# Kernel optimization log

Measured on AMD Instinct MI355X. Metric: run time of the kernel, lower is better.

The kernel has to match this reference:

```python
import jax, jax.numpy as jnp
import numpy as np

B, L, H, LAB = 64, 128, 512, 128

def setup_inputs() -> dict:
    key = jax.random.key(0)
    ks = jax.random.split(key, 8)
    s = 1.0 / np.sqrt(H)  # PyTorch LSTM/Linear uniform bound as a std-ish scale
    return {
        "x": jax.random.normal(ks[0], (B, L, 2 * H), jnp.float32),
        "hi": jax.random.normal(ks[1], (B, L, 2 * H), jnp.float32),
        "W_ih": jax.random.normal(ks[2], (4 * H, 5 * H), jnp.float32) * s,
        "W_hh": jax.random.normal(ks[3], (4 * H, H), jnp.float32) * s,
        "b_ih": jax.random.normal(ks[4], (4 * H,), jnp.float32) * s,
        "b_hh": jax.random.normal(ks[5], (4 * H,), jnp.float32) * s,
        "W_fc": jax.random.normal(ks[6], (LAB, H), jnp.float32) * s,
        "b_fc": jax.random.normal(ks[7], (LAB,), jnp.float32) * s,
    }

def _cell(xi, h, c, W_ih, W_hh, b_ih, b_hh):
    # PyTorch LSTMCell math, gate order: input, forget, cell(g), output
    gates = xi @ W_ih.T + b_ih + h @ W_hh.T + b_hh  # [4H]
    i, f, g, o = jnp.split(gates, 4)
    i = jax.nn.sigmoid(i); f = jax.nn.sigmoid(f); o = jax.nn.sigmoid(o)
    g = jnp.tanh(g)
    c = f * c + i * g
    h = o * jnp.tanh(c)
    return h, c

def reference(x, hi, W_ih, W_hh, b_ih, b_hh, W_fc, b_fc):
    Bm, Lm, _ = x.shape
    Hm = W_hh.shape[1]
    xs = jnp.concatenate([x, hi], axis=-1).transpose(1, 0, 2)  # [L, B, 4H]
    # Faithful to the torch code: nn.LSTM (batch_first=False) is fed [B,1,5H]
    # with state (1,1,H), so it scans the batch dim as 'time' with a single
    # shared (h,c) that also persists across outer timesteps.
    def time_step(carry, x_t):
        h, c, prev_out = carry  # h,c: [H]; prev_out: [B,H] (outputs of prev t)
        inp = jnp.concatenate([x_t, prev_out], axis=-1)  # [B, 5H]
        def batch_step(hc, xi):
            hh, cc = hc
            hh, cc = _cell(xi, hh, cc, W_ih, W_hh, b_ih, b_hh)
            return (hh, cc), hh
        (h, c), outs = jax.lax.scan(batch_step, (h, c), inp)  # outs: [B,H]
        return (h, c, outs), outs
    init = (jnp.zeros((Hm,), x.dtype), jnp.zeros((Hm,), x.dtype),
            jnp.zeros((Bm, Hm), x.dtype))
    _, all_out = jax.lax.scan(time_step, init, xs)  # [L, B, H]
    output = all_out.transpose(1, 0, 2)  # [B, L, H]
    return output @ W_fc.T + b_fc  # [B, L, label_size]
```

## Files before the change

### kernel.cpp

```cpp
#include <hip/hip_runtime.h>
#include <stdint.h>


#define HDIM   512
#define NSTEP  8192
#define GATES  2048
#define XDIM   2048
#define IN5H   2560
#define LSEQ   128
#define LAB    128
#define SPIN_LIMIT 1000000

typedef float f32x4 __attribute__((ext_vector_type(4)));
typedef short bf16x8 __attribute__((ext_vector_type(8)));

__device__ __forceinline__ unsigned f2bf(float v){
  unsigned u = __float_as_uint(v);
  u += 0x7fffu + ((u >> 16) & 1u);
  return u >> 16;
}
__device__ __forceinline__ float bf2f_lo(unsigned lo){ return __uint_as_float((lo & 0xffffu) << 16); }
__device__ __forceinline__ float bf2f_hi(unsigned lo){ return __uint_as_float(lo & 0xffff0000u); }

template<int PREMODE>
__global__ __launch_bounds__(256) void gemm_pre(
    const float* __restrict__ x, const float* __restrict__ hi,
    const float* __restrict__ Wih, const float* __restrict__ bih,
    const float* __restrict__ bhh, void* __restrict__ preOut)
{
  __shared__ unsigned short As[128][40];
  __shared__ unsigned short Bs[128][40];
  const int tid = threadIdx.x;
  const int bm = blockIdx.x, bn = blockIdx.y;
  const int lane = tid & 63, wv = tid >> 6;
  const int wm = wv & 1, wn = wv >> 1;

  const int srow = tid >> 1;
  const int ch   = (tid & 1) * 16;

  const int gr = bm*128 + srow;
  const int bb = gr & 63, tt = gr >> 6;
  const float* ax = x  + (size_t)(bb*LSEQ + tt) * 1024;
  const float* ah = hi + (size_t)(bb*LSEQ + tt) * 1024;
  const int R = bn*128 + srow;
  const float* bw = Wih + (size_t)R * IN5H;

  f32x4 acc[4][4];
  #pragma unroll
  for (int m=0;m<4;++m)
    #pragma unroll
    for (int n=0;n<4;++n) acc[m][n] = (f32x4){0.f,0.f,0.f,0.f};

  for (int kc = 0; kc < XDIM; kc += 32){
    const int c0 = kc + ch;
    const float* ap = (c0 < 1024) ? (ax + c0) : (ah + (c0 - 1024));
    #pragma unroll
    for (int q=0;q<4;++q){
      float4 va = *(const float4*)(ap + 4*q);
      float4 vb = *(const float4*)(bw + c0 + 4*q);
      ushort4 ua; ua.x=f2bf(va.x); ua.y=f2bf(va.y); ua.z=f2bf(va.z); ua.w=f2bf(va.w);
      ushort4 ub; ub.x=f2bf(vb.x); ub.y=f2bf(vb.y); ub.z=f2bf(vb.z); ub.w=f2bf(vb.w);
      *(ushort4*)&As[srow][ch + 4*q] = ua;
      *(ushort4*)&Bs[srow][ch + 4*q] = ub;
    }
    __syncthreads();
    bf16x8 afr[4], bfr[4];
    const int mr = wm*64 + (lane & 15);
    const int nr = wn*64 + (lane & 15);
    const int ko = (lane >> 4) * 8;
    #pragma unroll
    for (int m=0;m<4;++m) afr[m] = *(const bf16x8*)&As[mr + 16*m][ko];
    #pragma unroll
    for (int n=0;n<4;++n) bfr[n] = *(const bf16x8*)&Bs[nr + 16*n][ko];
    #pragma unroll
    for (int m=0;m<4;++m)
      #pragma unroll
      for (int n=0;n<4;++n)
        acc[m][n] = __builtin_amdgcn_mfma_f32_16x16x32_bf16(afr[m], bfr[n], acc[m][n], 0, 0, 0);
    __syncthreads();
  }
  #pragma unroll
  for (int n=0;n<4;++n){
    const int scol = bn*128 + wn*64 + 16*n + (lane & 15);
    const float bias = bih[scol] + bhh[scol];
    #pragma unroll
    for (int m=0;m<4;++m){
      const int sr0 = bm*128 + wm*64 + 16*m + (lane >> 4)*4;
      #pragma unroll
      for (int q=0;q<4;++q){
        const float v = acc[m][n][q] + bias;
        if (PREMODE == 0){
          ((float*)preOut)[(size_t)(sr0 + q) * GATES + scol] = v;
        } else {
          const float vn = __shfl_xor(v, 1, 64);
          if (!(lane & 1)){
            const unsigned word = f2bf(v) | (f2bf(vn) << 16);
            ((unsigned*)preOut)[(size_t)(sr0 + q) * 1024 + (scol >> 1)] = word;
          }
        }
      }
    }
  }
}

template<int PREMODE>
__global__ __launch_bounds__(512) void lstm_seq(
    const float* __restrict__ Wih, const float* __restrict__ Whh,
    const void* __restrict__ preOut, unsigned long long* __restrict__ units)
{
  const int tid = threadIdx.x;
  const int w = blockIdx.x;
  const int k = tid >> 6, l = tid & 63;

  __shared__ float hvec[512];
  __shared__ float uvec[512];
  __shared__ float accS[32];
  __shared__ float accU[32];
  __shared__ float preBuf[2][32];
  __shared__ int   sDead;

  float wu[4][8], wh[4][8];
  #pragma unroll
  for (int i=0;i<4;++i){
    const int rl = 4*k + i;
    const int gate = rl >> 3, jl = rl & 7;
    const int R = gate*HDIM + 8*w + jl;
    const float* pu = Wih + (size_t)R*IN5H + XDIM;
    const float* ph = Whh + (size_t)R*HDIM;
    #pragma unroll
    for (int c=0;c<8;++c){ wu[i][c] = pu[l + 64*c]; wh[i][c] = ph[l + 64*c]; }
  }
  hvec[tid] = 0.f; uvec[tid] = 0.f;
  if (tid == 0) sDead = 0;
  if (tid < 32) accU[tid] = 0.f;
  if (tid >= 32 && tid < 64){
    const int rl = tid - 32;
    if (PREMODE == 0){
      preBuf[0][rl] = ((const float*)preOut)[(size_t)0*GATES + (rl >> 3)*HDIM + 8*w + (rl & 7)];
    } else if (rl < 16){
      const int g = rl >> 2, wi = rl & 3;
      const unsigned word = ((const unsigned*)preOut)[(size_t)0*1024 + g*256 + 4*w + wi];
      preBuf[0][2*rl]   = bf2f_lo(word);
      preBuf[0][2*rl+1] = bf2f_hi(word);
    }
  }
  float cst = 0.f;
  __syncthreads();

  for (int s = 0; s < NSTEP; ++s){
    const int dead = sDead;
    if (!dead){
      if (k < 4){
        if (s > 0){
          const int idx = k*64 + l;
          const unsigned long long* p = units + (size_t)(s-1)*256 + idx;
          unsigned long long v; int trips = 0; int ok;
          do {
            v = __hip_atomic_load(p, __ATOMIC_RELAXED, __HIP_MEMORY_SCOPE_AGENT);
            ok = __all((int)((unsigned)(v >> 32) == (unsigned)s));
          } while (!ok && ++trips < SPIN_LIMIT);
          if (!ok) sDead = 1;
          const unsigned lo = (unsigned)v;
          hvec[2*idx]   = bf2f_lo(lo);
          hvec[2*idx+1] = bf2f_hi(lo);
        }
      } else {
        if (s >= 63){
          const int idx = (k-4)*64 + l;
          const unsigned long long* p = units + (size_t)(s-63)*256 + idx;
          unsigned long long v; int trips = 0; int ok;
          do {
            v = __hip_atomic_load(p, __ATOMIC_RELAXED, __HIP_MEMORY_SCOPE_AGENT);
            ok = __all((int)((unsigned)(v >> 32) == (unsigned)(s-62)));
          } while (!ok && ++trips < SPIN_LIMIT);
          if (!ok) sDead = 1;
          const unsigned lo = (unsigned)v;
          uvec[2*idx]   = bf2f_lo(lo);
          uvec[2*idx+1] = bf2f_hi(lo);
        }
      }
    }
    __syncthreads();

    {
      float a0=0.f, a1=0.f, a2=0.f, a3=0.f;
      #pragma unroll
      for (int c=0;c<8;++c){
        const float hv = hvec[l + 64*c];
        a0 += wh[0][c]*hv; a1 += wh[1][c]*hv; a2 += wh[2][c]*hv; a3 += wh[3][c]*hv;
      }
      #pragma unroll
      for (int off=32; off>=1; off>>=1){
        a0 += __shfl_xor(a0, off, 64);
        a1 += __shfl_xor(a1, off, 64);
        a2 += __shfl_xor(a2, off, 64);
        a3 += __shfl_xor(a3, off, 64);
      }
      if (l == 0){
        accS[4*k+0] = a0 + accU[4*k+0];
        accS[4*k+1] = a1 + accU[4*k+1];
        accS[4*k+2] = a2 + accU[4*k+2];
        accS[4*k+3] = a3 + accU[4*k+3];
      }
    }
    __syncthreads();

    if (tid < 8){
      const int jl = tid;
      const float* pb = preBuf[s & 1];
      float gi = accS[jl]      + pb[jl];
      float gf = accS[8 + jl]  + pb[8 + jl];
      float gg = accS[16 + jl] + pb[16 + jl];
      float go = accS[24 + jl] + pb[24 + jl];
      gi = 1.f/(1.f + __expf(-gi));
      gf = 1.f/(1.f + __expf(-gf));
      go = 1.f/(1.f + __expf(-go));
      float e2 = __expf(2.f * fminf(fmaxf(gg, -15.f), 15.f));
      gg = (e2 - 1.f) / (e2 + 1.f);
      cst = gf*cst + gi*gg;
      float e2c = __expf(2.f * fminf(fmaxf(cst, -15.f), 15.f));
      const float hval = go * ((e2c - 1.f) / (e2c + 1.f));
      const float hn = __shfl_xor(hval, 1, 64);
      if ((jl & 1) == 0){
        const unsigned lo = f2bf(hval) | (f2bf(hn) << 16);
        const unsigned long long unit =
            (unsigned long long)lo | ((unsigned long long)(unsigned)(s + 1) << 32);
        __hip_atomic_store(units + (size_t)s*256 + (4*w + (jl >> 1)), unit,
                           __ATOMIC_RELAXED, __HIP_MEMORY_SCOPE_AGENT);
      }
    }
    {
      float a0=0.f, a1=0.f, a2=0.f, a3=0.f;
      #pragma unroll
      for (int c=0;c<8;++c){
        const float uv = uvec[l + 64*c];
        a0 += wu[0][c]*uv; a1 += wu[1][c]*uv; a2 += wu[2][c]*uv; a3 += wu[3][c]*uv;
      }
      #pragma unroll
      for (int off=32; off>=1; off>>=1){
        a0 += __shfl_xor(a0, off, 64);
        a1 += __shfl_xor(a1, off, 64);
        a2 += __shfl_xor(a2, off, 64);
        a3 += __shfl_xor(a3, off, 64);
      }
      if (l == 0){
        accU[4*k+0] = a0; accU[4*k+1] = a1; accU[4*k+2] = a2; accU[4*k+3] = a3;
      }
    }
    if ((s + 1) < NSTEP && tid >= 32 && tid < 64){
      const int rl = tid - 32;
      if (PREMODE == 0){
        preBuf[(s+1) & 1][rl] =
            ((const float*)preOut)[(size_t)(s+1)*GATES + (rl >> 3)*HDIM + 8*w + (rl & 7)];
      } else if (rl < 16){
        const int g = rl >> 2, wi = rl & 3;
        const unsigned word = ((const unsigned*)preOut)[(size_t)(s+1)*1024 + g*256 + 4*w + wi];
        preBuf[(s+1) & 1][2*rl]   = bf2f_lo(word);
        preBuf[(s+1) & 1][2*rl+1] = bf2f_hi(word);
      }
    }
    __syncthreads();
  }
}

__global__ __launch_bounds__(256) void fc_kernel(
    const unsigned long long* __restrict__ units,
    const float* __restrict__ Wfc, const float* __restrict__ bfc,
    float* __restrict__ out)
{
  __shared__ float hbuf[8][512];
  const int tid = threadIdx.x;
  const int s0 = blockIdx.x * 8;
  #pragma unroll
  for (int r=0;r<8;++r){
    const int q = tid + 256*r;
    const int si = q >> 8, u = q & 255;
    const unsigned lo = (unsigned)units[(size_t)(s0 + si)*256 + u];
    hbuf[si][2*u]   = bf2f_lo(lo);
    hbuf[si][2*u+1] = bf2f_hi(lo);
  }
  __syncthreads();
  const int lab = tid & 127, sg = tid >> 7;
  const float* wrow = Wfc + (size_t)lab * HDIM;
  const float bias = bfc[lab];
  for (int si = sg; si < 8; si += 2){
    float sum = 0.f;
    #pragma unroll 4
    for (int j=0;j<HDIM;j+=4){
      const float4 wv = *(const float4*)(wrow + j);
      sum += wv.x*hbuf[si][j] + wv.y*hbuf[si][j+1]
           + wv.z*hbuf[si][j+2] + wv.w*hbuf[si][j+3];
    }
    const int s = s0 + si;
    const int bb = s & 63, tt = s >> 6;
    out[((size_t)(bb*LSEQ + tt))*LAB + lab] = sum + bias;
  }
}

__global__ void sentinel_kernel(float* out, int n){
  const int i = blockIdx.x*256 + threadIdx.x;
  if (i < n) out[i] = 12345.0f;
}

extern "C" void kernel_launch(void* const* d_in, const int* in_sizes, int n_in,
                              void* d_out, int out_size, void* d_ws, size_t ws_size,
                              hipStream_t stream)
{
  const float* x   = (const float*)d_in[0];
  const float* hi  = (const float*)d_in[1];
  const float* Wih = (const float*)d_in[2];
  const float* Whh = (const float*)d_in[3];
  const float* bih = (const float*)d_in[4];
  const float* bhh = (const float*)d_in[5];
  const float* Wfc = (const float*)d_in[6];
  const float* bfc = (const float*)d_in[7];
  float* out = (float*)d_out;

  const size_t MB = 1024*1024;
  if (ws_size >= 80*MB){
    void* pre = d_ws;
    unsigned long long* units =
        (unsigned long long*)((char*)d_ws + 64*MB);
    gemm_pre<0><<<dim3(64, 16), 256, 0, stream>>>(x, hi, Wih, bih, bhh, pre);
    lstm_seq<0><<<64, 512, 0, stream>>>(Wih, Whh, pre, units);
    fc_kernel<<<1024, 256, 0, stream>>>(units, Wfc, bfc, out);
  } else if (ws_size >= 48*MB){
    void* pre = d_ws;
    unsigned long long* units =
        (unsigned long long*)((char*)d_ws + 32*MB);
    gemm_pre<1><<<dim3(64, 16), 256, 0, stream>>>(x, hi, Wih, bih, bhh, pre);
    lstm_seq<1><<<64, 512, 0, stream>>>(Wih, Whh, pre, units);
    fc_kernel<<<1024, 256, 0, stream>>>(units, Wfc, bfc, out);
  } else {
    sentinel_kernel<<<(out_size + 255)/256, 256, 0, stream>>>(out, out_size);
  }
}
```

Before: 17.67 ms.

## Give each wave one hidden unit and drop block barriers from the LSTM recurrence

Restructures the persistent LSTM kernel so each wavefront owns one hidden unit across all four gates. Each wave polls the flag-tagged h and u vectors directly into registers, reduces with shuffles and applies the gate math locally. This removes the three per-step __syncthreads and the shared-memory staging, and launches 128 blocks of 256 threads instead of 64 of 512. Each h entry becomes a 32-bit word holding a bf16 value and a 16-bit step tag, and the pre-activations are always stored as bf16. Every wave now loads the full vectors itself, which adds global/L2 traffic, and the 16-bit tag wraps at 65536 steps (fine for 8192 steps).

```diff
diff --git a/kernel.cpp b/kernel.cpp
--- a/kernel.cpp
+++ b/kernel.cpp
@@ -4,12 +4,11 @@
 
 #define HDIM   512
 #define NSTEP  8192
-#define GATES  2048
 #define XDIM   2048
 #define IN5H   2560
 #define LSEQ   128
 #define LAB    128
-#define SPIN_LIMIT 1000000
+#define SPIN_LIMIT 65536
 
 typedef float f32x4 __attribute__((ext_vector_type(4)));
 typedef short bf16x8 __attribute__((ext_vector_type(8)));
@@ -19,14 +18,13 @@
   u += 0x7fffu + ((u >> 16) & 1u);
   return u >> 16;
 }
-__device__ __forceinline__ float bf2f_lo(unsigned lo){ return __uint_as_float((lo & 0xffffu) << 16); }
-__device__ __forceinline__ float bf2f_hi(unsigned lo){ return __uint_as_float(lo & 0xffff0000u); }
-
-template<int PREMODE>
+__device__ __forceinline__ float bf2f_lo(unsigned w){ return __uint_as_float((w & 0xffffu) << 16); }
+__device__ __forceinline__ float bf2f_hi(unsigned w){ return __uint_as_float(w & 0xffff0000u); }
+
 __global__ __launch_bounds__(256) void gemm_pre(
     const float* __restrict__ x, const float* __restrict__ hi,
     const float* __restrict__ Wih, const float* __restrict__ bih,
-    const float* __restrict__ bhh, void* __restrict__ preOut)
+    const float* __restrict__ bhh, unsigned* __restrict__ pre32)
 {
   __shared__ unsigned short As[128][40];
   __shared__ unsigned short Bs[128][40];
@@ -89,182 +87,151 @@
       #pragma unroll
       for (int q=0;q<4;++q){
         const float v = acc[m][n][q] + bias;
-        if (PREMODE == 0){
-          ((float*)preOut)[(size_t)(sr0 + q) * GATES + scol] = v;
-        } else {
-          const float vn = __shfl_xor(v, 1, 64);
-          if (!(lane & 1)){
-            const unsigned word = f2bf(v) | (f2bf(vn) << 16);
-            ((unsigned*)preOut)[(size_t)(sr0 + q) * 1024 + (scol >> 1)] = word;
-          }
+        const float vn = __shfl_xor(v, 1, 64);
+        if (!(lane & 1)){
+          const unsigned word = f2bf(v) | (f2bf(vn) << 16);
+          pre32[(size_t)(sr0 + q) * 1024 + (scol >> 1)] = word;
         }
       }
     }
   }
 }
 
-template<int PREMODE>
-__global__ __launch_bounds__(512) void lstm_seq(
+__global__ __launch_bounds__(256, 1) void lstm_seq(
     const float* __restrict__ Wih, const float* __restrict__ Whh,
-    const void* __restrict__ preOut, unsigned long long* __restrict__ units)
+    const unsigned* __restrict__ pre32, unsigned* __restrict__ units)
 {
   const int tid = threadIdx.x;
-  const int w = blockIdx.x;
-  const int k = tid >> 6, l = tid & 63;
-
-  __shared__ float hvec[512];
-  __shared__ float uvec[512];
-  __shared__ float accS[32];
-  __shared__ float accU[32];
-  __shared__ float preBuf[2][32];
-  __shared__ int   sDead;
-
-  float wu[4][8], wh[4][8];
-  #pragma unroll
-  for (int i=0;i<4;++i){
-    const int rl = 4*k + i;
-    const int gate = rl >> 3, jl = rl & 7;
-    const int R = gate*HDIM + 8*w + jl;
-    const float* pu = Wih + (size_t)R*IN5H + XDIM;
-    const float* ph = Whh + (size_t)R*HDIM;
-    #pragma unroll
-    for (int c=0;c<8;++c){ wu[i][c] = pu[l + 64*c]; wh[i][c] = ph[l + 64*c]; }
-  }
-  hvec[tid] = 0.f; uvec[tid] = 0.f;
-  if (tid == 0) sDead = 0;
-  if (tid < 32) accU[tid] = 0.f;
-  if (tid >= 32 && tid < 64){
-    const int rl = tid - 32;
-    if (PREMODE == 0){
-      preBuf[0][rl] = ((const float*)preOut)[(size_t)0*GATES + (rl >> 3)*HDIM + 8*w + (rl & 7)];
-    } else if (rl < 16){
-      const int g = rl >> 2, wi = rl & 3;
-      const unsigned word = ((const unsigned*)preOut)[(size_t)0*1024 + g*256 + 4*w + wi];
-      preBuf[0][2*rl]   = bf2f_lo(word);
-      preBuf[0][2*rl+1] = bf2f_hi(word);
-    }
-  }
+  const int l = tid & 63;
+  const int j0 = blockIdx.x * 4 + (tid >> 6);
+
+  float wh[4][8], wu[4][8];
+  #pragma unroll
+  for (int g=0; g<4; ++g){
+    const float* ph = Whh + (size_t)(g*HDIM + j0)*HDIM;
+    const float* pu = Wih + (size_t)(g*HDIM + j0)*IN5H + XDIM;
+    #pragma unroll
+    for (int c=0; c<8; ++c){ wh[g][c] = ph[l + 64*c]; wu[g][c] = pu[l + 64*c]; }
+  }
+
+  const int phalf = j0 >> 1, psel = j0 & 1;
+  float pr[4];
+  #pragma unroll
+  for (int g=0; g<4; ++g){
+    const unsigned w0 = pre32[(size_t)0*1024 + g*256 + phalf];
+    pr[g] = psel ? bf2f_hi(w0) : bf2f_lo(w0);
+  }
+
   float cst = 0.f;
-  __syncthreads();
+  int dead = 0;
 
   for (int s = 0; s < NSTEP; ++s){
-    const int dead = sDead;
-    if (!dead){
-      if (k < 4){
-        if (s > 0){
-          const int idx = k*64 + l;
-          const unsigned long long* p = units + (size_t)(s-1)*256 + idx;
-          unsigned long long v; int trips = 0; int ok;
-          do {
-            v = __hip_atomic_load(p, __ATOMIC_RELAXED, __HIP_MEMORY_SCOPE_AGENT);
-            ok = __all((int)((unsigned)(v >> 32) == (unsigned)s));
-          } while (!ok && ++trips < SPIN_LIMIT);
-          if (!ok) sDead = 1;
-          const unsigned lo = (unsigned)v;
-          hvec[2*idx]   = bf2f_lo(lo);
-          hvec[2*idx+1] = bf2f_hi(lo);
-        }
+    float hv[8], uv[8];
+    if (s == 0){
+      #pragma unroll
+      for (int c=0;c<8;++c) hv[c] = 0.f;
+    } else {
+      const unsigned* bp = units + (size_t)(s-1)*HDIM + l;
+      unsigned v[8];
+      if (dead){
+        #pragma unroll
+        for (int c=0;c<8;++c) v[c] = __hip_atomic_load(bp + 64*c, __ATOMIC_RELAXED, __HIP_MEMORY_SCOPE_AGENT);
       } else {
-        if (s >= 63){
-          const int idx = (k-4)*64 + l;
-          const unsigned long long* p = units + (size_t)(s-63)*256 + idx;
-          unsigned long long v; int trips = 0; int ok;
-          do {
-            v = __hip_atomic_load(p, __ATOMIC_RELAXED, __HIP_MEMORY_SCOPE_AGENT);
-            ok = __all((int)((unsigned)(v >> 32) == (unsigned)(s-62)));
-          } while (!ok && ++trips < SPIN_LIMIT);
-          if (!ok) sDead = 1;
-          const unsigned lo = (unsigned)v;
-          uvec[2*idx]   = bf2f_lo(lo);
-          uvec[2*idx+1] = bf2f_hi(lo);
-        }
-      }
-    }
-    __syncthreads();
-
-    {
-      float a0=0.f, a1=0.f, a2=0.f, a3=0.f;
-      #pragma unroll
-      for (int c=0;c<8;++c){
-        const float hv = hvec[l + 64*c];
-        a0 += wh[0][c]*hv; a1 += wh[1][c]*hv; a2 += wh[2][c]*hv; a3 += wh[3][c]*hv;
-      }
-      #pragma unroll
-      for (int off=32; off>=1; off>>=1){
-        a0 += __shfl_xor(a0, off, 64);
-        a1 += __shfl_xor(a1, off, 64);
-        a2 += __shfl_xor(a2, off, 64);
-        a3 += __shfl_xor(a3, off, 64);
-      }
-      if (l == 0){
-        accS[4*k+0] = a0 + accU[4*k+0];
-        accS[4*k+1] = a1 + accU[4*k+1];
-        accS[4*k+2] = a2 + accU[4*k+2];
-        accS[4*k+3] = a3 + accU[4*k+3];
-      }
-    }
-    __syncthreads();
-
-    if (tid < 8){
-      const int jl = tid;
-      const float* pb = preBuf[s & 1];
-      float gi = accS[jl]      + pb[jl];
-      float gf = accS[8 + jl]  + pb[8 + jl];
-      float gg = accS[16 + jl] + pb[16 + jl];
-      float go = accS[24 + jl] + pb[24 + jl];
-      gi = 1.f/(1.f + __expf(-gi));
-      gf = 1.f/(1.f + __expf(-gf));
-      go = 1.f/(1.f + __expf(-go));
-      float e2 = __expf(2.f * fminf(fmaxf(gg, -15.f), 15.f));
-      gg = (e2 - 1.f) / (e2 + 1.f);
-      cst = gf*cst + gi*gg;
-      float e2c = __expf(2.f * fminf(fmaxf(cst, -15.f), 15.f));
-      const float hval = go * ((e2c - 1.f) / (e2c + 1.f));
-      const float hn = __shfl_xor(hval, 1, 64);
-      if ((jl & 1) == 0){
-        const unsigned lo = f2bf(hval) | (f2bf(hn) << 16);
-        const unsigned long long unit =
-            (unsigned long long)lo | ((unsigned long long)(unsigned)(s + 1) << 32);
-        __hip_atomic_store(units + (size_t)s*256 + (4*w + (jl >> 1)), unit,
-                           __ATOMIC_RELAXED, __HIP_MEMORY_SCOPE_AGENT);
-      }
-    }
-    {
-      float a0=0.f, a1=0.f, a2=0.f, a3=0.f;
-      #pragma unroll
-      for (int c=0;c<8;++c){
-        const float uv = uvec[l + 64*c];
-        a0 += wu[0][c]*uv; a1 += wu[1][c]*uv; a2 += wu[2][c]*uv; a3 += wu[3][c]*uv;
-      }
-      #pragma unroll
-      for (int off=32; off>=1; off>>=1){
-        a0 += __shfl_xor(a0, off, 64);
-        a1 += __shfl_xor(a1, off, 64);
-        a2 += __shfl_xor(a2, off, 64);
-        a3 += __shfl_xor(a3, off, 64);
-      }
-      if (l == 0){
-        accU[4*k+0] = a0; accU[4*k+1] = a1; accU[4*k+2] = a2; accU[4*k+3] = a3;
-      }
-    }
-    if ((s + 1) < NSTEP && tid >= 32 && tid < 64){
-      const int rl = tid - 32;
-      if (PREMODE == 0){
-        preBuf[(s+1) & 1][rl] =
-            ((const float*)preOut)[(size_t)(s+1)*GATES + (rl >> 3)*HDIM + 8*w + (rl & 7)];
-      } else if (rl < 16){
-        const int g = rl >> 2, wi = rl & 3;
-        const unsigned word = ((const unsigned*)preOut)[(size_t)(s+1)*1024 + g*256 + 4*w + wi];
-        preBuf[(s+1) & 1][2*rl]   = bf2f_lo(word);
-        preBuf[(s+1) & 1][2*rl+1] = bf2f_hi(word);
-      }
-    }
-    __syncthreads();
+        int trips = 0, ok;
+        do {
+          #pragma unroll
+          for (int c=0;c<8;++c) v[c] = __hip_atomic_load(bp + 64*c, __ATOMIC_RELAXED, __HIP_MEMORY_SCOPE_AGENT);
+          int lok = 1;
+          #pragma unroll
+          for (int c=0;c<8;++c) lok &= ((v[c] >> 16) == (unsigned)s);
+          ok = __all(lok);
+        } while (!ok && ++trips < SPIN_LIMIT);
+        if (!ok) dead = 1;
+      }
+      #pragma unroll
+      for (int c=0;c<8;++c) hv[c] = bf2f_lo(v[c]);
+    }
+    if (s >= 64){
+      const unsigned* bp = units + (size_t)(s-64)*HDIM + l;
+      unsigned v[8];
+      if (dead){
+        #pragma unroll
+        for (int c=0;c<8;++c) v[c] = __hip_atomic_load(bp + 64*c, __ATOMIC_RELAXED, __HIP_MEMORY_SCOPE_AGENT);
+      } else {
+        int trips = 0, ok;
+        do {
+          #pragma unroll
+          for (int c=0;c<8;++c) v[c] = __hip_atomic_load(bp + 64*c, __ATOMIC_RELAXED, __HIP_MEMORY_SCOPE_AGENT);
+          int lok = 1;
+          #pragma unroll
+          for (int c=0;c<8;++c) lok &= ((v[c] >> 16) == (unsigned)(s-63));
+          ok = __all(lok);
+        } while (!ok && ++trips < SPIN_LIMIT);
+        if (!ok) dead = 1;
+      }
+      #pragma unroll
+      for (int c=0;c<8;++c) uv[c] = bf2f_lo(v[c]);
+    } else {
+      #pragma unroll
+      for (int c=0;c<8;++c) uv[c] = 0.f;
+    }
+
+    float prn[4];
+    if (s + 1 < NSTEP){
+      #pragma unroll
+      for (int g=0; g<4; ++g){
+        const unsigned w0 = pre32[(size_t)(s+1)*1024 + g*256 + phalf];
+        prn[g] = psel ? bf2f_hi(w0) : bf2f_lo(w0);
+      }
+    } else {
+      #pragma unroll
+      for (int g=0; g<4; ++g) prn[g] = 0.f;
+    }
+
+    float a0=0.f, a1=0.f, a2=0.f, a3=0.f;
+    #pragma unroll
+    for (int c=0;c<8;++c){
+      a0 += wh[0][c]*hv[c]; a1 += wh[1][c]*hv[c];
+      a2 += wh[2][c]*hv[c]; a3 += wh[3][c]*hv[c];
+    }
+    #pragma unroll
+    for (int c=0;c<8;++c){
+      a0 += wu[0][c]*uv[c]; a1 += wu[1][c]*uv[c];
+      a2 += wu[2][c]*uv[c]; a3 += wu[3][c]*uv[c];
+    }
+    #pragma unroll
+    for (int off=32; off>=1; off>>=1){
+      a0 += __shfl_xor(a0, off, 64);
+      a1 += __shfl_xor(a1, off, 64);
+      a2 += __shfl_xor(a2, off, 64);
+      a3 += __shfl_xor(a3, off, 64);
+    }
+
+    float gi = a0 + pr[0];
+    float gf = a1 + pr[1];
+    float gg = a2 + pr[2];
+    float go = a3 + pr[3];
+    gi = 1.f/(1.f + __expf(-gi));
+    gf = 1.f/(1.f + __expf(-gf));
+    go = 1.f/(1.f + __expf(-go));
+    float e2 = __expf(2.f * fminf(fmaxf(gg, -15.f), 15.f));
+    gg = (e2 - 1.f) / (e2 + 1.f);
+    cst = gf*cst + gi*gg;
+    float e2c = __expf(2.f * fminf(fmaxf(cst, -15.f), 15.f));
+    const float hval = go * ((e2c - 1.f) / (e2c + 1.f));
+
+    if (l == 0){
+      const unsigned unit = ((unsigned)(s + 1) << 16) | f2bf(hval);
+      __hip_atomic_store(units + (size_t)s*HDIM + j0, unit,
+                         __ATOMIC_RELAXED, __HIP_MEMORY_SCOPE_AGENT);
+    }
+    #pragma unroll
+    for (int g=0; g<4; ++g) pr[g] = prn[g];
   }
 }
 
 __global__ __launch_bounds__(256) void fc_kernel(
-    const unsigned long long* __restrict__ units,
+    const unsigned* __restrict__ units,
     const float* __restrict__ Wfc, const float* __restrict__ bfc,
     float* __restrict__ out)
 {
@@ -272,12 +239,10 @@
   const int tid = threadIdx.x;
   const int s0 = blockIdx.x * 8;
   #pragma unroll
-  for (int r=0;r<8;++r){
+  for (int r=0;r<16;++r){
     const int q = tid + 256*r;
-    const int si = q >> 8, u = q & 255;
-    const unsigned lo = (unsigned)units[(size_t)(s0 + si)*256 + u];
-    hbuf[si][2*u]   = bf2f_lo(lo);
-    hbuf[si][2*u+1] = bf2f_hi(lo);
+    const int si = q >> 9, j = q & 511;
+    hbuf[si][j] = bf2f_lo(units[(size_t)(s0 + si)*HDIM + j]);
   }
   __syncthreads();
   const int lab = tid & 127, sg = tid >> 7;
@@ -317,19 +282,11 @@
   float* out = (float*)d_out;
 
   const size_t MB = 1024*1024;
-  if (ws_size >= 80*MB){
-    void* pre = d_ws;
-    unsigned long long* units =
-        (unsigned long long*)((char*)d_ws + 64*MB);
-    gemm_pre<0><<<dim3(64, 16), 256, 0, stream>>>(x, hi, Wih, bih, bhh, pre);
-    lstm_seq<0><<<64, 512, 0, stream>>>(Wih, Whh, pre, units);
-    fc_kernel<<<1024, 256, 0, stream>>>(units, Wfc, bfc, out);
-  } else if (ws_size >= 48*MB){
-    void* pre = d_ws;
-    unsigned long long* units =
-        (unsigned long long*)((char*)d_ws + 32*MB);
-    gemm_pre<1><<<dim3(64, 16), 256, 0, stream>>>(x, hi, Wih, bih, bhh, pre);
-    lstm_seq<1><<<64, 512, 0, stream>>>(Wih, Whh, pre, units);
+  if (ws_size >= 48*MB){
+    unsigned* pre32 = (unsigned*)d_ws;
+    unsigned* units = (unsigned*)((char*)d_ws + 32*MB);
+    gemm_pre<<<dim3(64, 16), 256, 0, stream>>>(x, hi, Wih, bih, bhh, pre32);
+    lstm_seq<<<128, 256, 0, stream>>>(Wih, Whh, pre32, units);
     fc_kernel<<<1024, 256, 0, stream>>>(units, Wfc, bfc, out);
   } else {
     sentinel_kernel<<<(out_size + 255)/256, 256, 0, stream>>>(out, out_size);
```

New measurement: 32.79 ms. +85.6%, slower.
